# Performance work log

Measured on AMD Instinct MI355X. Metric: run time of the kernel, lower is better.

## Reference

```python
import jax, jax.numpy as jnp
import numpy as np

N, E, H, Q, M, B, L = 100000, 800000, 64, 4, 8, 100, 4
EPS_BN = 1e-5


def setup_inputs() -> dict:
    key = jax.random.key(0)
    ki = iter(jax.random.split(key, 32))
    def nrm(shape, scale=1.0):
        return jax.random.normal(next(ki), shape, dtype=jnp.float32) * scale
    inp = {}
    inp["x"] = nrm((N, H))
    inp["pe"] = nrm((N, Q, M, 2))
    inp["Lam"] = jax.random.uniform(next(ki), (B, Q, M), jnp.float32, 0.0, 2.0)
    inp["edge_attr"] = nrm((E, H))
    # per-layer eigenvalue MLP phi: scalar -> 16 -> scalar
    inp["phi_w1"] = nrm((L, 1, 16))
    inp["phi_b1"] = jnp.zeros((L, 16), jnp.float32)
    inp["phi_w2"] = nrm((L, 16, 1), 0.25)
    inp["phi_b2"] = jnp.zeros((L, 1), jnp.float32)
    # per-layer edge PE encoder linear: [2*Q*M -> H]
    inp["enc_w"] = nrm((L, 2 * Q * M, H), (2.0 / (2 * Q * M)) ** 0.5)
    inp["enc_b"] = jnp.zeros((L, H), jnp.float32)
    # per-layer GINE edge linear
    inp["lin_w"] = nrm((L, H, H), (2.0 / H) ** 0.5)
    inp["lin_b"] = jnp.zeros((L, H), jnp.float32)
    # per-layer GINE MLP: Linear -> BN -> ReLU -> Linear
    inp["mlp_w1"] = nrm((L, H, H), (2.0 / H) ** 0.5)
    inp["mlp_b1"] = jnp.zeros((L, H), jnp.float32)
    inp["bn1_g"] = jnp.ones((L, H), jnp.float32)
    inp["bn1_b"] = jnp.zeros((L, H), jnp.float32)
    inp["mlp_w2"] = nrm((L, H, H), (2.0 / H) ** 0.5)
    inp["mlp_b2"] = jnp.zeros((L, H), jnp.float32)
    # per-layer outer BatchNorm
    inp["bn2_g"] = jnp.ones((L, H), jnp.float32)
    inp["bn2_b"] = jnp.zeros((L, H), jnp.float32)
    inp["edge_index"] = jax.random.randint(next(ki), (2, E), 0, N, dtype=jnp.int32)
    inp["batch"] = jnp.sort(jax.random.randint(next(ki), (N,), 0, B, dtype=jnp.int32))
    return inp


def _bn(h, g, b):
    # training-mode BatchNorm1d over the node/row axis
    mu = h.mean(axis=0)
    var = h.var(axis=0)
    return (h - mu) * jax.lax.rsqrt(var + EPS_BN) * g + b


def _forward(x, pe, Lam, edge_attr, params, edge_index, batch):
    (phi_w1, phi_b1, phi_w2, phi_b2, enc_w, enc_b, lin_w, lin_b,
     mlp_w1, mlp_b1, bn1_g, bn1_b, mlp_w2, mlp_b2, bn2_g, bn2_b) = params
    src, dst = edge_index[0], edge_index[1]
    # permutation-invariant complex edge features: pe[src] * conj(pe[dst]), per (q, eigvec)
    zs_re, zs_im = pe[src, ..., 0], pe[src, ..., 1]   # [E, Q, M]
    zd_re, zd_im = pe[dst, ..., 0], pe[dst, ..., 1]
    z_re = zs_re * zd_re + zs_im * zd_im              # [E, Q, M]
    z_im = zs_im * zd_re - zs_re * zd_im
    eg = batch[src]                                    # graph id per edge  [E]
    for l in range(L):
        # eigenvalue MLP -> per-eigenvector weight  [B, Q, M]
        hphi = jax.nn.relu(Lam[..., None] @ phi_w1[l] + phi_b1[l])   # [B,Q,M,16]
        w = (hphi @ phi_w2[l])[..., 0] + phi_b2[l][0]                # [B,Q,M]
        we = w[eg]                                                   # [E,Q,M]
        feat = jnp.concatenate([(z_re * we).reshape(E, Q * M),
                                (z_im * we).reshape(E, Q * M)], axis=-1)  # [E, 2QM]
        edge_pe = feat @ enc_w[l] + enc_b[l]                          # [E,H]
        ea = edge_pe + edge_attr
        # GINE message: ReLU(x_j + lin(edge_attr)), sum-aggregated at dst
        msg = jax.nn.relu(x[src] + ea @ lin_w[l] + lin_b[l])          # [E,H]
        agg = jax.ops.segment_sum(msg, dst, num_segments=N)           # [N,H]
        h = x + agg                                                   # (1+eps)*x with eps=0
        h = jax.nn.relu(_bn(h @ mlp_w1[l] + mlp_b1[l], bn1_g[l], bn1_b[l]))
        h = h @ mlp_w2[l] + mlp_b2[l]
        x = _bn(h, bn2_g[l], bn2_b[l])
        if l != L - 1:
            x = jax.nn.relu(x)
    return x


def reference(x, pe, Lam, edge_attr, phi_w1, phi_b1, phi_w2, phi_b2, enc_w, enc_b,
              lin_w, lin_b, mlp_w1, mlp_b1, bn1_g, bn1_b, mlp_w2, mlp_b2, bn2_g, bn2_b,
              edge_index, batch):
    params = (phi_w1, phi_b1, phi_w2, phi_b2, enc_w, enc_b, lin_w, lin_b,
              mlp_w1, mlp_b1, bn1_g, bn1_b, mlp_w2, mlp_b2, bn2_g, bn2_b)
    return (_forward(x, pe, Lam, edge_attr, params, edge_index, batch), pe)
```

## Files before the change

### kernel.cpp

```cpp
#include <hip/hip_runtime.h>

#define N_NODES 100000
#define N_EDGES 800000
#define NB 100
#define NL 4
#define QM 32
#define EPS_BN 1e-5f

typedef __bf16 bf16_t;
typedef __bf16 bf16x8 __attribute__((ext_vector_type(8)));
typedef __bf16 bf16x4 __attribute__((ext_vector_type(4)));
typedef __bf16 bf16x2 __attribute__((ext_vector_type(2)));
typedef float f32x4 __attribute__((ext_vector_type(4)));


__global__ void k_count(const int* __restrict__ dst, int* __restrict__ counts) {
    int e = blockIdx.x * 256 + threadIdx.x;
    if (e < N_EDGES) atomicAdd(&counts[dst[e]], 1);
}

__global__ void k_scan1(const int* __restrict__ counts, int* __restrict__ row_ptr,
                        int* __restrict__ blk) {
    __shared__ int s[1024];
    int i = blockIdx.x * 1024 + threadIdx.x;
    int v = (i < N_NODES) ? counts[i] : 0;
    s[threadIdx.x] = v;
    __syncthreads();
    for (int off = 1; off < 1024; off <<= 1) {
        int u = (threadIdx.x >= off) ? s[threadIdx.x - off] : 0;
        __syncthreads();
        s[threadIdx.x] += u;
        __syncthreads();
    }
    if (i < N_NODES) row_ptr[i] = s[threadIdx.x] - v;
    if (threadIdx.x == 1023) blk[blockIdx.x] = s[1023];
}

__global__ void k_scan2(int* __restrict__ blk) {
    __shared__ int s[128];
    int t = threadIdx.x;
    int v = (t < 98) ? blk[t] : 0;
    s[t] = v;
    __syncthreads();
    for (int off = 1; off < 128; off <<= 1) {
        int u = (t >= off) ? s[t - off] : 0;
        __syncthreads();
        s[t] += u;
        __syncthreads();
    }
    if (t < 98) blk[t] = s[t] - v;
}

__global__ void k_scan3(const int* __restrict__ blk, int* __restrict__ row_ptr) {
    int i = blockIdx.x * 1024 + threadIdx.x;
    if (i < N_NODES) row_ptr[i] += blk[blockIdx.x];
    if (i == 0) row_ptr[N_NODES] = N_EDGES;
}

__global__ void k_scatter(const int* __restrict__ ei, const int* __restrict__ batch,
                          const int* __restrict__ row_ptr, int* __restrict__ cursor,
                          int4* __restrict__ edat) {
    int e = blockIdx.x * 256 + threadIdx.x;
    if (e >= N_EDGES) return;
    int s = ei[e], d = ei[N_EDGES + e];
    int pos = row_ptr[d] + atomicAdd(&cursor[d], 1);
    edat[pos] = make_int4(s, d, batch[s], e);
}

__global__ void k_permute(const float* __restrict__ pe, const float* __restrict__ ea,
                          const int4* __restrict__ edat, bf16_t* __restrict__ feat) {
    int t = blockIdx.x * 256 + threadIdx.x;
    int p = t >> 4, k = t & 15;
    int4 ed = edat[p];
    int src = ed.x, dst = ed.y, e = ed.w;
    f32x4 av = *(const f32x4*)(ea + (size_t)e * 64 + k * 4);
    bf16x4 ao;
#pragma unroll
    for (int i = 0; i < 4; i++) ao[i] = (bf16_t)av[i];
    *(bf16x4*)(feat + (size_t)p * 128 + 64 + k * 4) = ao;
    f32x4 sv = *(const f32x4*)(pe + (size_t)src * 64 + k * 4);
    f32x4 dv = *(const f32x4*)(pe + (size_t)dst * 64 + k * 4);
    bf16x2 re, im;
    re[0] = (bf16_t)(sv[0] * dv[0] + sv[1] * dv[1]);
    re[1] = (bf16_t)(sv[2] * dv[2] + sv[3] * dv[3]);
    im[0] = (bf16_t)(sv[1] * dv[0] - sv[0] * dv[1]);
    im[1] = (bf16_t)(sv[3] * dv[2] - sv[2] * dv[3]);
    *(bf16x2*)(feat + (size_t)p * 128 + 2 * k) = re;
    *(bf16x2*)(feat + (size_t)p * 128 + 32 + 2 * k) = im;
}


__global__ void k_phi(const float* __restrict__ Lam, const float* __restrict__ w1,
                      const float* __restrict__ b1, const float* __restrict__ w2,
                      const float* __restrict__ b2, bf16_t* __restrict__ w_all) {
    int idx = blockIdx.x * 256 + threadIdx.x;
    if (idx >= NL * NB * QM) return;
    int l = idx / (NB * QM);
    int rem = idx % (NB * QM);
    float lam = Lam[rem];
    float acc = b2[l];
    for (int i = 0; i < 16; i++) {
        float h = lam * w1[l * 16 + i] + b1[l * 16 + i];
        acc += fmaxf(h, 0.f) * w2[l * 16 + i];
    }
    w_all[idx] = (bf16_t)acc;
}

__global__ void k_prep(const float* __restrict__ enc_w, const float* __restrict__ enc_b,
                       const float* __restrict__ lin_w, const float* __restrict__ lin_b,
                       const float* __restrict__ mlp_w1, const float* __restrict__ mlp_w2,
                       bf16_t* __restrict__ wcat_frag, bf16_t* __restrict__ w1frag,
                       bf16_t* __restrict__ w2frag, float* __restrict__ cvec) {
    __shared__ float lds[128][64];
    int l = blockIdx.x, tid = threadIdx.x;
    const float* ew = enc_w + l * 64 * 64;
    const float* lw = lin_w + l * 64 * 64;
    for (int idx = tid; idx < 64 * 64; idx += 256) {
        int r = idx >> 6, c = idx & 63;
        float acc = 0.f;
        for (int k = 0; k < 64; k++) acc += ew[r * 64 + k] * lw[k * 64 + c];
        lds[r][c] = acc;
        lds[64 + r][c] = lw[r * 64 + c];
    }
    if (tid < 64) {
        float acc = lin_b[l * 64 + tid];
        for (int k = 0; k < 64; k++) acc += enc_b[l * 64 + k] * lw[k * 64 + tid];
        cvec[l * 64 + tid] = acc;
    }
    __syncthreads();
    for (int idx = tid; idx < 16 * 512; idx += 256) {
        int sn = idx >> 9, lane = (idx >> 3) & 63, j = idx & 7;
        int s = sn >> 2, nt = sn & 3;
        int row = 32 * s + (lane >> 4) * 8 + j;
        int col = 16 * nt + (lane & 15);
        wcat_frag[l * 8192 + idx] = (bf16_t)lds[row][col];
    }
    for (int idx = tid; idx < 8 * 512; idx += 256) {
        int sn = idx >> 9, lane = (idx >> 3) & 63, j = idx & 7;
        int s = sn >> 2, nt = sn & 3;
        int row = 32 * s + (lane >> 4) * 8 + j;
        int col = 16 * nt + (lane & 15);
        w1frag[l * 4096 + idx] = (bf16_t)mlp_w1[(l * 64 + row) * 64 + col];
        w2frag[l * 4096 + idx] = (bf16_t)mlp_w2[(l * 64 + row) * 64 + col];
    }
}


__global__ void k_hinit0(const float* __restrict__ x, bf16_t* __restrict__ x_bf,
                         float* __restrict__ h) {
    size_t i = ((size_t)blockIdx.x * 256 + threadIdx.x) * 8;
    f32x4 a = *(const f32x4*)(x + i), b = *(const f32x4*)(x + i + 4);
    *(f32x4*)(h + i) = a;
    *(f32x4*)(h + i + 4) = b;
    bf16x8 o;
#pragma unroll
    for (int k = 0; k < 4; k++) { o[k] = (bf16_t)a[k]; o[k + 4] = (bf16_t)b[k]; }
    *(bf16x8*)(x_bf + i) = o;
}

__global__ void k_edge(const bf16_t* __restrict__ feat, const int4* __restrict__ edat,
                       const int* __restrict__ row_ptr, const bf16_t* __restrict__ w_l,
                       const bf16_t* __restrict__ wcat_l, const float* __restrict__ cvec_l,
                       const bf16_t* __restrict__ x_bf, float* __restrict__ h) {
    __shared__ float msg[128][68];
    int tid = threadIdx.x;
    int wave = tid >> 6, lane = tid & 63;
    int quad = lane >> 4, l16 = lane & 15;
    int e0 = blockIdx.x * 128;

    bf16x8 bfrag[4][4];
    const bf16x8* wf = (const bf16x8*)wcat_l;
#pragma unroll
    for (int s = 0; s < 4; s++)
#pragma unroll
        for (int nt = 0; nt < 4; nt++) bfrag[s][nt] = wf[(s * 4 + nt) * 64 + lane];

    f32x4 acc[2][4];
#pragma unroll
    for (int rt = 0; rt < 2; rt++)
#pragma unroll
        for (int nt = 0; nt < 4; nt++) acc[rt][nt] = (f32x4)(0.f);

    int em[2];
    bf16x8 wch[2];
#pragma unroll
    for (int rt = 0; rt < 2; rt++) {
        em[rt] = e0 + wave * 32 + rt * 16 + l16;
        int eg = edat[em[rt]].z;
        wch[rt] = *(const bf16x8*)(w_l + (size_t)eg * QM + quad * 8);
    }
#pragma unroll
    for (int s = 0; s < 4; s++) {
        bf16x8 afr[2];
#pragma unroll
        for (int rt = 0; rt < 2; rt++) {
            bf16x8 v = *(const bf16x8*)(feat + (size_t)em[rt] * 128 + s * 32 + quad * 8);
            if (s < 2) {
                bf16x8 a;
#pragma unroll
                for (int i = 0; i < 8; i++) a[i] = (bf16_t)((float)v[i] * (float)wch[rt][i]);
                afr[rt] = a;
            } else {
                afr[rt] = v;
            }
        }
#pragma unroll
        for (int rt = 0; rt < 2; rt++)
#pragma unroll
            for (int nt = 0; nt < 4; nt++)
                acc[rt][nt] = __builtin_amdgcn_mfma_f32_16x16x32_bf16(afr[rt], bfrag[s][nt],
                                                                     acc[rt][nt], 0, 0, 0);
    }
#pragma unroll
    for (int nt = 0; nt < 4; nt++) {
        float cv = cvec_l[nt * 16 + l16];
#pragma unroll
        for (int rt = 0; rt < 2; rt++)
#pragma unroll
            for (int r = 0; r < 4; r++)
                msg[wave * 32 + rt * 16 + quad * 4 + r][nt * 16 + l16] = acc[rt][nt][r] + cv;
    }
    __syncthreads();
#pragma unroll
    for (int it = 0; it < 4; it++) {
        int j = it * 32 + (tid >> 3);
        int l8 = tid & 7;
        int srcn = edat[e0 + j].x;
        bf16x8 xv = *(const bf16x8*)(x_bf + (size_t)srcn * 64 + l8 * 8);
        float* mrow = &msg[j][l8 * 8];
        f32x4 m0 = *(const f32x4*)mrow, m1 = *(const f32x4*)(mrow + 4);
#pragma unroll
        for (int k = 0; k < 4; k++) {
            m0[k] = fmaxf(m0[k] + (float)xv[k], 0.f);
            m1[k] = fmaxf(m1[k] + (float)xv[k + 4], 0.f);
        }
        *(f32x4*)mrow = m0;
        *(f32x4*)(mrow + 4) = m1;
    }
    __syncthreads();
    int nfirst = edat[e0].y, nlast = edat[e0 + 127].y;
    int c = tid & 63;
    for (int n = nfirst + (tid >> 6); n <= nlast; n += 4) {
        int rs = row_ptr[n], re = row_ptr[n + 1];
        int a = rs > e0 ? rs : e0;
        int b = re < e0 + 128 ? re : e0 + 128;
        if (a >= b) continue;
        float sum = 0.f;
        for (int jj = a; jj < b; jj++) sum += msg[jj - e0][c];
        float* addr = h + (size_t)n * 64 + c;
        if (rs >= e0 && re <= e0 + 128) *addr += sum;
        else atomicAdd(addr, sum);
    }
}

__global__ void k_mlp1(const float* __restrict__ h, const bf16_t* __restrict__ w1frag_l,
                       const float* __restrict__ b1_l, bf16_t* __restrict__ t,
                       float* __restrict__ stats) {
    __shared__ float sred[128];
    int tid = threadIdx.x, wave = tid >> 6, lane = tid & 63, quad = lane >> 4, l16 = lane & 15;
    int r0 = blockIdx.x * 128;
    bf16x8 bfrag[2][4];
    const bf16x8* wf = (const bf16x8*)w1frag_l;
#pragma unroll
    for (int s = 0; s < 2; s++)
#pragma unroll
        for (int nt = 0; nt < 4; nt++) bfrag[s][nt] = wf[(s * 4 + nt) * 64 + lane];
    f32x4 acc[2][4];
#pragma unroll
    for (int rt = 0; rt < 2; rt++)
#pragma unroll
        for (int nt = 0; nt < 4; nt++) acc[rt][nt] = (f32x4)(0.f);
#pragma unroll
    for (int rt = 0; rt < 2; rt++) {
        int n = r0 + wave * 32 + rt * 16 + l16;
        bool valid = n < N_NODES;
#pragma unroll
        for (int s = 0; s < 2; s++) {
            bf16x8 a;
            if (valid) {
                const float* hp = h + (size_t)n * 64 + s * 32 + quad * 8;
                f32x4 v0 = *(const f32x4*)hp, v1 = *(const f32x4*)(hp + 4);
#pragma unroll
                for (int i = 0; i < 4; i++) { a[i] = (bf16_t)v0[i]; a[i + 4] = (bf16_t)v1[i]; }
            } else {
#pragma unroll
                for (int i = 0; i < 8; i++) a[i] = (bf16_t)0.f;
            }
#pragma unroll
            for (int nt = 0; nt < 4; nt++)
                acc[rt][nt] = __builtin_amdgcn_mfma_f32_16x16x32_bf16(a, bfrag[s][nt],
                                                                     acc[rt][nt], 0, 0, 0);
        }
    }
    if (tid < 128) sred[tid] = 0.f;
    __syncthreads();
#pragma unroll
    for (int nt = 0; nt < 4; nt++) {
        int col = nt * 16 + l16;
        float bias = b1_l[col];
        float s1 = 0.f, s2 = 0.f;
#pragma unroll
        for (int rt = 0; rt < 2; rt++)
#pragma unroll
            for (int r = 0; r < 4; r++) {
                int n = r0 + wave * 32 + rt * 16 + quad * 4 + r;
                if (n < N_NODES) {
                    float v = acc[rt][nt][r] + bias;
                    t[(size_t)n * 64 + col] = (bf16_t)v;
                    s1 += v; s2 += v * v;
                }
            }
        s1 += __shfl_xor(s1, 16); s1 += __shfl_xor(s1, 32);
        s2 += __shfl_xor(s2, 16); s2 += __shfl_xor(s2, 32);
        if (quad == 0) { atomicAdd(&sred[col], s1); atomicAdd(&sred[64 + col], s2); }
    }
    __syncthreads();
    if (tid < 128) atomicAdd(&stats[tid], sred[tid]);
}

__global__ void k_mlp2(const bf16_t* __restrict__ t, const float* __restrict__ stats1,
                       const float* __restrict__ g1, const float* __restrict__ b1,
                       const bf16_t* __restrict__ w2frag_l, const float* __restrict__ b2_l,
                       float* __restrict__ h2, float* __restrict__ stats2) {
    __shared__ float sred[128];
    __shared__ float cf[128];
    int tid = threadIdx.x, wave = tid >> 6, lane = tid & 63, quad = lane >> 4, l16 = lane & 15;
    int r0 = blockIdx.x * 128;
    bf16x8 bfrag[2][4];
    const bf16x8* wf = (const bf16x8*)w2frag_l;
#pragma unroll
    for (int s = 0; s < 2; s++)
#pragma unroll
        for (int nt = 0; nt < 4; nt++) bfrag[s][nt] = wf[(s * 4 + nt) * 64 + lane];
    if (tid < 64) {
        float mean = stats1[tid] / (float)N_NODES;
        float var = stats1[64 + tid] / (float)N_NODES - mean * mean;
        float a = g1[tid] * rsqrtf(var + EPS_BN);
        cf[tid] = a;
        cf[64 + tid] = b1[tid] - mean * a;
    }
    if (tid >= 64 && tid < 192) sred[tid - 64] = 0.f;
    __syncthreads();
    f32x4 acc[2][4];
#pragma unroll
    for (int rt = 0; rt < 2; rt++)
#pragma unroll
        for (int nt = 0; nt < 4; nt++) acc[rt][nt] = (f32x4)(0.f);
#pragma unroll
    for (int rt = 0; rt < 2; rt++) {
        int n = r0 + wave * 32 + rt * 16 + l16;
        bool valid = n < N_NODES;
#pragma unroll
        for (int s = 0; s < 2; s++) {
            bf16x8 a;
            if (valid) {
                bf16x8 tv = *(const bf16x8*)(t + (size_t)n * 64 + s * 32 + quad * 8);
                int kb = s * 32 + quad * 8;
#pragma unroll
                for (int i = 0; i < 8; i++) {
                    float y = (float)tv[i] * cf[kb + i] + cf[64 + kb + i];
                    a[i] = (bf16_t)fmaxf(y, 0.f);
                }
            } else {
#pragma unroll
                for (int i = 0; i < 8; i++) a[i] = (bf16_t)0.f;
            }
#pragma unroll
            for (int nt = 0; nt < 4; nt++)
                acc[rt][nt] = __builtin_amdgcn_mfma_f32_16x16x32_bf16(a, bfrag[s][nt],
                                                                     acc[rt][nt], 0, 0, 0);
        }
    }
#pragma unroll
    for (int nt = 0; nt < 4; nt++) {
        int col = nt * 16 + l16;
        float bias = b2_l[col];
        float s1 = 0.f, s2 = 0.f;
#pragma unroll
        for (int rt = 0; rt < 2; rt++)
#pragma unroll
            for (int r = 0; r < 4; r++) {
                int n = r0 + wave * 32 + rt * 16 + quad * 4 + r;
                if (n < N_NODES) {
                    float v = acc[rt][nt][r] + bias;
                    h2[(size_t)n * 64 + col] = v;
                    s1 += v; s2 += v * v;
                }
            }
        s1 += __shfl_xor(s1, 16); s1 += __shfl_xor(s1, 32);
        s2 += __shfl_xor(s2, 16); s2 += __shfl_xor(s2, 32);
        if (quad == 0) { atomicAdd(&sred[col], s1); atomicAdd(&sred[64 + col], s2); }
    }
    __syncthreads();
    if (tid < 128) atomicAdd(&stats2[tid], sred[tid]);
}

__global__ void k_apply_init(const float* __restrict__ h2, const float* __restrict__ stats2,
                             const float* __restrict__ g, const float* __restrict__ b,
                             bf16_t* __restrict__ x_bf, float* __restrict__ h) {
    __shared__ float cf[128];
    int tid = threadIdx.x;
    if (tid < 64) {
        float mean = stats2[tid] / (float)N_NODES;
        float var = stats2[64 + tid] / (float)N_NODES - mean * mean;
        float a = g[tid] * rsqrtf(var + EPS_BN);
        cf[tid] = a;
        cf[64 + tid] = b[tid] - mean * a;
    }
    __syncthreads();
    size_t i = ((size_t)blockIdx.x * 256 + tid) * 8;
    int c0 = (int)(i & 63);
    f32x4 v0 = *(const f32x4*)(h2 + i), v1 = *(const f32x4*)(h2 + i + 4);
    f32x4 y0, y1;
    bf16x8 o;
#pragma unroll
    for (int k = 0; k < 4; k++) {
        y0[k] = fmaxf(v0[k] * cf[c0 + k] + cf[64 + c0 + k], 0.f);
        y1[k] = fmaxf(v1[k] * cf[c0 + 4 + k] + cf[64 + c0 + 4 + k], 0.f);
        o[k] = (bf16_t)y0[k]; o[k + 4] = (bf16_t)y1[k];
    }
    *(f32x4*)(h + i) = y0;
    *(f32x4*)(h + i + 4) = y1;
    *(bf16x8*)(x_bf + i) = o;
}

__global__ void k_apply_out(const float* __restrict__ h2, const float* __restrict__ stats2,
                            const float* __restrict__ g, const float* __restrict__ b,
                            float* __restrict__ out) {
    __shared__ float cf[128];
    int tid = threadIdx.x;
    if (tid < 64) {
        float mean = stats2[tid] / (float)N_NODES;
        float var = stats2[64 + tid] / (float)N_NODES - mean * mean;
        float a = g[tid] * rsqrtf(var + EPS_BN);
        cf[tid] = a;
        cf[64 + tid] = b[tid] - mean * a;
    }
    __syncthreads();
    size_t i = ((size_t)blockIdx.x * 256 + tid) * 8;
    int c0 = (int)(i & 63);
    f32x4 v0 = *(const f32x4*)(h2 + i), v1 = *(const f32x4*)(h2 + i + 4);
    f32x4 y0, y1;
#pragma unroll
    for (int k = 0; k < 4; k++) {
        y0[k] = v0[k] * cf[c0 + k] + cf[64 + c0 + k];
        y1[k] = v1[k] * cf[c0 + 4 + k] + cf[64 + c0 + 4 + k];
    }
    *(f32x4*)(out + i) = y0;
    *(f32x4*)(out + i + 4) = y1;
}


extern "C" void kernel_launch(void* const* d_in, const int* in_sizes, int n_in,
                              void* d_out, int out_size, void* d_ws, size_t ws_size,
                              hipStream_t stream) {
    const float* x_in   = (const float*)d_in[0];
    const float* pe     = (const float*)d_in[1];
    const float* Lam    = (const float*)d_in[2];
    const float* eattr  = (const float*)d_in[3];
    const float* phi_w1 = (const float*)d_in[4];
    const float* phi_b1 = (const float*)d_in[5];
    const float* phi_w2 = (const float*)d_in[6];
    const float* phi_b2 = (const float*)d_in[7];
    const float* enc_w  = (const float*)d_in[8];
    const float* enc_b  = (const float*)d_in[9];
    const float* lin_w  = (const float*)d_in[10];
    const float* lin_b  = (const float*)d_in[11];
    const float* mlp_w1 = (const float*)d_in[12];
    const float* mlp_b1 = (const float*)d_in[13];
    const float* bn1_g  = (const float*)d_in[14];
    const float* bn1_b  = (const float*)d_in[15];
    const float* mlp_w2 = (const float*)d_in[16];
    const float* mlp_b2 = (const float*)d_in[17];
    const float* bn2_g  = (const float*)d_in[18];
    const float* bn2_b  = (const float*)d_in[19];
    const int* edge_index = (const int*)d_in[20];
    const int* batch      = (const int*)d_in[21];
    float* out = (float*)d_out;

    char* ws = (char*)d_ws;
    size_t off = 0;
    auto alloc = [&](size_t bytes) -> void* {
        void* p = ws + off;
        off += (bytes + 255) & ~(size_t)255;
        return p;
    };
    bf16_t* feat      = (bf16_t*)alloc((size_t)N_EDGES * 128 * 2);
    int4* edat        = (int4*)alloc((size_t)N_EDGES * 16);
    int* row_ptr      = (int*)alloc((size_t)(N_NODES + 1) * 4);
    int* blk          = (int*)alloc(128 * 4);
    int* counts       = (int*)alloc((size_t)N_NODES * 4);
    int* cursor       = (int*)alloc((size_t)N_NODES * 4);
    float* stats      = (float*)alloc((size_t)NL * 256 * 4);
    size_t zbytes     = (char*)(stats + NL * 256) - (char*)counts;
    float* h          = (float*)alloc((size_t)N_NODES * 64 * 4);
    bf16_t* t         = (bf16_t*)alloc((size_t)N_NODES * 64 * 2);
    float* h2         = (float*)alloc((size_t)N_NODES * 64 * 4);
    bf16_t* x_bf      = (bf16_t*)alloc((size_t)N_NODES * 64 * 2);
    bf16_t* w_all     = (bf16_t*)alloc((size_t)NL * NB * QM * 2);
    bf16_t* wcat_frag = (bf16_t*)alloc((size_t)NL * 8192 * 2);
    bf16_t* w1frag    = (bf16_t*)alloc((size_t)NL * 4096 * 2);
    bf16_t* w2frag    = (bf16_t*)alloc((size_t)NL * 4096 * 2);
    float* cvec       = (float*)alloc((size_t)NL * 64 * 4);

    hipMemsetAsync(counts, 0, zbytes, stream);
    k_count<<<3125, 256, 0, stream>>>(edge_index + N_EDGES, counts);
    k_scan1<<<98, 1024, 0, stream>>>(counts, row_ptr, blk);
    k_scan2<<<1, 128, 0, stream>>>(blk);
    k_scan3<<<98, 1024, 0, stream>>>(blk, row_ptr);
    k_scatter<<<3125, 256, 0, stream>>>(edge_index, batch, row_ptr, cursor, edat);
    k_permute<<<50000, 256, 0, stream>>>(pe, eattr, edat, feat);
    k_phi<<<50, 256, 0, stream>>>(Lam, phi_w1, phi_b1, phi_w2, phi_b2, w_all);
    k_prep<<<NL, 256, 0, stream>>>(enc_w, enc_b, lin_w, lin_b, mlp_w1, mlp_w2,
                                   wcat_frag, w1frag, w2frag, cvec);

    k_hinit0<<<3125, 256, 0, stream>>>(x_in, x_bf, h);
    for (int l = 0; l < NL; l++) {
        float* s1 = stats + l * 256;
        float* s2 = stats + l * 256 + 128;
        k_edge<<<6250, 256, 0, stream>>>(feat, edat, row_ptr,
                                         w_all + (size_t)l * NB * QM,
                                         wcat_frag + (size_t)l * 8192,
                                         cvec + (size_t)l * 64, x_bf, h);
        k_mlp1<<<782, 256, 0, stream>>>(h, w1frag + (size_t)l * 4096,
                                        mlp_b1 + l * 64, t, s1);
        k_mlp2<<<782, 256, 0, stream>>>(t, s1, bn1_g + l * 64, bn1_b + l * 64,
                                        w2frag + (size_t)l * 4096, mlp_b2 + l * 64,
                                        h2, s2);
        if (l < NL - 1)
            k_apply_init<<<3125, 256, 0, stream>>>(h2, s2, bn2_g + l * 64, bn2_b + l * 64,
                                                   x_bf, h);
        else
            k_apply_out<<<3125, 256, 0, stream>>>(h2, s2, bn2_g + l * 64, bn2_b + l * 64,
                                                  out);
    }
    hipMemcpyAsync(out + (size_t)N_NODES * 64, pe, (size_t)N_NODES * QM * 2 * 4,
                   hipMemcpyDeviceToDevice, stream);
}
```

Baseline: 1.194 ms.

## Recompute PE edge products inside edge kernel instead of materializing them

```diff
diff --git a/kernel.cpp b/kernel.cpp
--- a/kernel.cpp
+++ b/kernel.cpp
@@ -9,8 +9,6 @@
 
 typedef __bf16 bf16_t;
 typedef __bf16 bf16x8 __attribute__((ext_vector_type(8)));
-typedef __bf16 bf16x4 __attribute__((ext_vector_type(4)));
-typedef __bf16 bf16x2 __attribute__((ext_vector_type(2)));
 typedef float f32x4 __attribute__((ext_vector_type(4)));
 
 
@@ -67,26 +65,17 @@
     edat[pos] = make_int4(s, d, batch[s], e);
 }
 
-__global__ void k_permute(const float* __restrict__ pe, const float* __restrict__ ea,
-                          const int4* __restrict__ edat, bf16_t* __restrict__ feat) {
+__global__ void k_permute(const float* __restrict__ ea, const int4* __restrict__ edat,
+                          bf16_t* __restrict__ ea_s) {
     int t = blockIdx.x * 256 + threadIdx.x;
-    int p = t >> 4, k = t & 15;
-    int4 ed = edat[p];
-    int src = ed.x, dst = ed.y, e = ed.w;
-    f32x4 av = *(const f32x4*)(ea + (size_t)e * 64 + k * 4);
-    bf16x4 ao;
-#pragma unroll
-    for (int i = 0; i < 4; i++) ao[i] = (bf16_t)av[i];
-    *(bf16x4*)(feat + (size_t)p * 128 + 64 + k * 4) = ao;
-    f32x4 sv = *(const f32x4*)(pe + (size_t)src * 64 + k * 4);
-    f32x4 dv = *(const f32x4*)(pe + (size_t)dst * 64 + k * 4);
-    bf16x2 re, im;
-    re[0] = (bf16_t)(sv[0] * dv[0] + sv[1] * dv[1]);
-    re[1] = (bf16_t)(sv[2] * dv[2] + sv[3] * dv[3]);
-    im[0] = (bf16_t)(sv[1] * dv[0] - sv[0] * dv[1]);
-    im[1] = (bf16_t)(sv[3] * dv[2] - sv[2] * dv[3]);
-    *(bf16x2*)(feat + (size_t)p * 128 + 2 * k) = re;
-    *(bf16x2*)(feat + (size_t)p * 128 + 32 + 2 * k) = im;
+    int p = t >> 3, k = t & 7;
+    int e = edat[p].w;
+    const float* ap = ea + (size_t)e * 64 + k * 8;
+    f32x4 a0 = *(const f32x4*)ap, a1 = *(const f32x4*)(ap + 4);
+    bf16x8 o;
+#pragma unroll
+    for (int i = 0; i < 4; i++) { o[i] = (bf16_t)a0[i]; o[i + 4] = (bf16_t)a1[i]; }
+    *(bf16x8*)(ea_s + (size_t)p * 64 + k * 8) = o;
 }
 
 
@@ -158,11 +147,13 @@
     *(bf16x8*)(x_bf + i) = o;
 }
 
-__global__ void k_edge(const bf16_t* __restrict__ feat, const int4* __restrict__ edat,
-                       const int* __restrict__ row_ptr, const bf16_t* __restrict__ w_l,
-                       const bf16_t* __restrict__ wcat_l, const float* __restrict__ cvec_l,
-                       const bf16_t* __restrict__ x_bf, float* __restrict__ h) {
+__global__ void k_edge(const float* __restrict__ pe, const bf16_t* __restrict__ ea_s,
+                       const int4* __restrict__ edat, const int* __restrict__ row_ptr,
+                       const bf16_t* __restrict__ w_l, const bf16_t* __restrict__ wcat_l,
+                       const float* __restrict__ cvec_l, const bf16_t* __restrict__ x_bf,
+                       float* __restrict__ h) {
     __shared__ float msg[128][68];
+    __shared__ int src_sh[128];
     int tid = threadIdx.x;
     int wave = tid >> 6, lane = tid & 63;
     int quad = lane >> 4, l16 = lane & 15;
@@ -181,28 +172,46 @@
 #pragma unroll
         for (int nt = 0; nt < 4; nt++) acc[rt][nt] = (f32x4)(0.f);
 
-    int em[2];
+    int em[2], srcv[2], dstv[2];
     bf16x8 wch[2];
 #pragma unroll
     for (int rt = 0; rt < 2; rt++) {
         em[rt] = e0 + wave * 32 + rt * 16 + l16;
-        int eg = edat[em[rt]].z;
-        wch[rt] = *(const bf16x8*)(w_l + (size_t)eg * QM + quad * 8);
+        int4 ed = edat[em[rt]];
+        srcv[rt] = ed.x; dstv[rt] = ed.y;
+        wch[rt] = *(const bf16x8*)(w_l + (size_t)ed.z * QM + quad * 8);
+        if (quad == 0) src_sh[em[rt] - e0] = ed.x;
+    }
+    bf16x8 afr_re[2], afr_im[2];
+#pragma unroll
+    for (int rt = 0; rt < 2; rt++) {
+        const f32x4* ps = (const f32x4*)(pe + (size_t)srcv[rt] * 64 + quad * 16);
+        const f32x4* pd = (const f32x4*)(pe + (size_t)dstv[rt] * 64 + quad * 16);
+        f32x4 s0 = ps[0], s1 = ps[1], s2 = ps[2], s3 = ps[3];
+        f32x4 d0 = pd[0], d1 = pd[1], d2 = pd[2], d3 = pd[3];
+        float sv[16], dv[16];
+#pragma unroll
+        for (int i = 0; i < 4; i++) {
+            sv[i] = s0[i]; sv[4 + i] = s1[i]; sv[8 + i] = s2[i]; sv[12 + i] = s3[i];
+            dv[i] = d0[i]; dv[4 + i] = d1[i]; dv[8 + i] = d2[i]; dv[12 + i] = d3[i];
+        }
+#pragma unroll
+        for (int j = 0; j < 8; j++) {
+            float sr = sv[2 * j], si = sv[2 * j + 1];
+            float dr = dv[2 * j], di = dv[2 * j + 1];
+            float w = (float)wch[rt][j];
+            afr_re[rt][j] = (bf16_t)((sr * dr + si * di) * w);
+            afr_im[rt][j] = (bf16_t)((si * dr - sr * di) * w);
+        }
     }
 #pragma unroll
     for (int s = 0; s < 4; s++) {
         bf16x8 afr[2];
 #pragma unroll
         for (int rt = 0; rt < 2; rt++) {
-            bf16x8 v = *(const bf16x8*)(feat + (size_t)em[rt] * 128 + s * 32 + quad * 8);
-            if (s < 2) {
-                bf16x8 a;
-#pragma unroll
-                for (int i = 0; i < 8; i++) a[i] = (bf16_t)((float)v[i] * (float)wch[rt][i]);
-                afr[rt] = a;
-            } else {
-                afr[rt] = v;
-            }
+            if (s == 0) afr[rt] = afr_re[rt];
+            else if (s == 1) afr[rt] = afr_im[rt];
+            else afr[rt] = *(const bf16x8*)(ea_s + (size_t)em[rt] * 64 + (s - 2) * 32 + quad * 8);
         }
 #pragma unroll
         for (int rt = 0; rt < 2; rt++)
@@ -225,7 +234,7 @@
     for (int it = 0; it < 4; it++) {
         int j = it * 32 + (tid >> 3);
         int l8 = tid & 7;
-        int srcn = edat[e0 + j].x;
+        int srcn = src_sh[j];
         bf16x8 xv = *(const bf16x8*)(x_bf + (size_t)srcn * 64 + l8 * 8);
         float* mrow = &msg[j][l8 * 8];
         f32x4 m0 = *(const f32x4*)mrow, m1 = *(const f32x4*)(mrow + 4);
@@ -485,7 +494,7 @@
         off += (bytes + 255) & ~(size_t)255;
         return p;
     };
-    bf16_t* feat      = (bf16_t*)alloc((size_t)N_EDGES * 128 * 2);
+    bf16_t* ea_s      = (bf16_t*)alloc((size_t)N_EDGES * 64 * 2);
     int4* edat        = (int4*)alloc((size_t)N_EDGES * 16);
     int* row_ptr      = (int*)alloc((size_t)(N_NODES + 1) * 4);
     int* blk          = (int*)alloc(128 * 4);
@@ -509,7 +518,7 @@
     k_scan2<<<1, 128, 0, stream>>>(blk);
     k_scan3<<<98, 1024, 0, stream>>>(blk, row_ptr);
     k_scatter<<<3125, 256, 0, stream>>>(edge_index, batch, row_ptr, cursor, edat);
-    k_permute<<<50000, 256, 0, stream>>>(pe, eattr, edat, feat);
+    k_permute<<<25000, 256, 0, stream>>>(eattr, edat, ea_s);
     k_phi<<<50, 256, 0, stream>>>(Lam, phi_w1, phi_b1, phi_w2, phi_b2, w_all);
     k_prep<<<NL, 256, 0, stream>>>(enc_w, enc_b, lin_w, lin_b, mlp_w1, mlp_w2,
                                    wcat_frag, w1frag, w2frag, cvec);
@@ -518,7 +527,7 @@
     for (int l = 0; l < NL; l++) {
         float* s1 = stats + l * 256;
         float* s2 = stats + l * 256 + 128;
-        k_edge<<<6250, 256, 0, stream>>>(feat, edat, row_ptr,
+        k_edge<<<6250, 256, 0, stream>>>(pe, ea_s, edat, row_ptr,
                                          w_all + (size_t)l * NB * QM,
                                          wcat_frag + (size_t)l * 8192,
                                          cvec + (size_t)l * 64, x_bf, h);
```

Measured after the change: 1.206 ms. Within noise of the previous version (+1.0%).
